# Kernel optimization log

Measured on AMD Instinct MI355X. Metric: run time of the kernel, lower is better.

## Reference

```python
import jax, jax.numpy as jnp
import numpy as np
import math

B, S, D, H, NL, DFF, C, K = 32, 1024, 512, 8, 6, 2048, 128, 8
HD = D // H  # head_dim = 64
EPS = 1e-5


def setup_inputs() -> dict:
    key = jax.random.key(0)
    ks = jax.random.split(key, 24)
    n = lambda k, shape, s=0.02: jax.random.normal(k, shape, jnp.float32) * s
    return {
        'theta': jax.random.uniform(ks[0], (B, S), jnp.float32, -math.pi, math.pi),
        'cond': jax.random.normal(ks[1], (B, C), jnp.float32),
        'attn_bias': jax.random.normal(ks[2], (H, S, S), jnp.float32) * 0.1,
        'embed_W': n(ks[3], (2, D)), 'embed_b': jnp.zeros((D,), jnp.float32),
        'ln1_g': jnp.ones((NL, D), jnp.float32), 'ln1_b': jnp.zeros((NL, D), jnp.float32),
        'ada1_W': n(ks[4], (NL, C, 2 * D)), 'ada1_b': jnp.zeros((NL, 2 * D), jnp.float32),
        'Wq': n(ks[5], (NL, D, D)), 'bq': jnp.zeros((NL, D), jnp.float32),
        'Wk': n(ks[6], (NL, D, D)), 'bk': jnp.zeros((NL, D), jnp.float32),
        'Wv': n(ks[7], (NL, D, D)), 'bv': jnp.zeros((NL, D), jnp.float32),
        'Wo': n(ks[8], (NL, D, D)), 'bo': jnp.zeros((NL, D), jnp.float32),
        'ln2_g': jnp.ones((NL, D), jnp.float32), 'ln2_b': jnp.zeros((NL, D), jnp.float32),
        'ada2_W': n(ks[9], (NL, C, 2 * D)), 'ada2_b': jnp.zeros((NL, 2 * D), jnp.float32),
        'W1': n(ks[10], (NL, D, DFF)), 'b1': jnp.zeros((NL, DFF), jnp.float32),
        'W2': n(ks[11], (NL, DFF, D)), 'b2': jnp.zeros((NL, D), jnp.float32),
        'fn_g': jnp.ones((D,), jnp.float32), 'fn_b': jnp.zeros((D,), jnp.float32),
        'head_W': n(ks[12], (D, 3 * K)), 'head_b': jnp.zeros((3 * K,), jnp.float32),
    }


def _layer_norm(x, g, b):
    m = jnp.mean(x, axis=-1, keepdims=True)
    v = jnp.mean(jnp.square(x - m), axis=-1, keepdims=True)
    return (x - m) * jax.lax.rsqrt(v + EPS) * g + b


def _adaln(x, cond, g, b, pW, pb):
    # AdaLN(x, c) = (1 + scale(c)) * LN(x) + shift(c)
    ss = cond @ pW + pb                      # [B, 2D]
    scale, shift = jnp.split(ss, 2, axis=-1)  # each [B, D]
    return (1.0 + scale[:, None, :]) * _layer_norm(x, g, b) + shift[:, None, :]


def reference(theta, cond, attn_bias, embed_W, embed_b, ln1_g, ln1_b, ada1_W, ada1_b,
              Wq, bq, Wk, bk, Wv, bv, Wo, bo, ln2_g, ln2_b, ada2_W, ada2_b,
              W1, b1, W2, b2, fn_g, fn_b, head_W, head_b):
    b_sz, s_len = theta.shape
    # circular embedding: (cos, sin) -> d_model
    emb_in = jnp.stack([jnp.cos(theta), jnp.sin(theta)], axis=-1)  # [B, S, 2]
    x = emb_in @ embed_W + embed_b                                 # [B, S, D]
    causal = jnp.triu(jnp.ones((s_len, s_len), bool), k=1)         # True above diag
    neg_inf = jnp.asarray(-jnp.inf, x.dtype)
    inv_sqrt = 1.0 / math.sqrt(HD)
    for i in range(NL):
        h = _adaln(x, cond, ln1_g[i], ln1_b[i], ada1_W[i], ada1_b[i])
        q = (h @ Wq[i] + bq[i]).reshape(b_sz, s_len, H, HD)
        k = (h @ Wk[i] + bk[i]).reshape(b_sz, s_len, H, HD)
        v = (h @ Wv[i] + bv[i]).reshape(b_sz, s_len, H, HD)
        scores = jnp.einsum('bqhd,bkhd->bhqk', q, k) * inv_sqrt  # [B, H, S, S]
        scores = scores + attn_bias[None]
        scores = jnp.where(causal[None, None], neg_inf, scores)
        attn = jax.nn.softmax(scores, axis=-1)
        ao = jnp.einsum('bhqk,bkhd->bqhd', attn, v).reshape(b_sz, s_len, D)
        x = x + (ao @ Wo[i] + bo[i])
        h2 = _adaln(x, cond, ln2_g[i], ln2_b[i], ada2_W[i], ada2_b[i])
        ff = jax.nn.gelu(h2 @ W1[i] + b1[i], approximate=False) @ W2[i] + b2[i]
        x = x + ff
    x = _layer_norm(x, fn_g, fn_b)
    return x @ head_W + head_b  # [B, S, 3K] mixture params (logw, mu, log-kappa)
```

## Files before the change

### kernel.cpp

```cpp
#include <hip/hip_runtime.h>


typedef short s8v __attribute__((ext_vector_type(8)));
typedef float f4v __attribute__((ext_vector_type(4)));
typedef unsigned u2v __attribute__((ext_vector_type(2)));
typedef unsigned u4v __attribute__((ext_vector_type(4)));

#define Q_SCALE 0.18033688011112042f
#define LOG2E   1.4426950408889634f

static __device__ __forceinline__ short f2bf(float f) {
  union { float f; unsigned u; } v; v.f = f;
  unsigned r = v.u + 0x7fffu + ((v.u >> 16) & 1u);
  return (short)(r >> 16);
}
static __device__ __forceinline__ float bf2f(unsigned short s) {
  union { unsigned u; float f; } v; v.u = ((unsigned)s) << 16;
  return v.f;
}
static __device__ __forceinline__ unsigned cvtpk(float lo, float hi) {
  unsigned r;
  asm("v_cvt_pk_bf16_f32 %0, %1, %2" : "=v"(r) : "v"(lo), "v"(hi));
  return r;
}
static __device__ __forceinline__ float fexp2(float x) {
  float r;
  asm("v_exp_f32 %0, %1" : "=v"(r) : "v"(x));
  return r;
}
static __device__ __forceinline__ void gl_lds16(const short* g, short* l) {
  __builtin_amdgcn_global_load_lds(
      (const __attribute__((address_space(1))) unsigned int*)g,
      (__attribute__((address_space(3))) unsigned int*)l, 16, 0, 0);
}

__global__ void transpose_all_k(const float* __restrict__ Wq, const float* __restrict__ Wk,
                                const float* __restrict__ Wv, const float* __restrict__ Wo,
                                const float* __restrict__ W1, const float* __restrict__ W2,
                                int l, short* __restrict__ wbf) {
  int id = blockIdx.x;
  const float* in; short* out; int K, N, tx, ty;
  if (id < 1024) {
    int m = id >> 8, t = id & 255;
    in = (m == 0 ? Wq : m == 1 ? Wk : m == 2 ? Wv : Wo) + (size_t)l * 262144;
    out = wbf + (size_t)m * 262144;
    K = 512; N = 512; tx = t & 15; ty = t >> 4;
  } else if (id < 2048) {
    int t = id - 1024;
    in = W1 + (size_t)l * 1048576; out = wbf + 1048576;
    K = 512; N = 2048; tx = t & 63; ty = t >> 6;
  } else {
    int t = id - 2048;
    in = W2 + (size_t)l * 1048576; out = wbf + 2097152;
    K = 2048; N = 512; tx = t & 15; ty = t >> 4;
  }
  __shared__ float tb[32][33];
  int n0 = tx * 32, k0 = ty * 32;
  int cx = threadIdx.x & 31, cy = threadIdx.x >> 5;
#pragma unroll
  for (int r = 0; r < 4; r++)
    tb[cy + r * 8][cx] = in[(size_t)(k0 + cy + r * 8) * N + n0 + cx];
  __syncthreads();
#pragma unroll
  for (int r = 0; r < 4; r++)
    out[(size_t)(n0 + cy + r * 8) * K + k0 + cx] = f2bf(tb[cx][cy + r * 8]);
}

__global__ void bias_cvt_k(const float* __restrict__ in, short* __restrict__ out) {
  int i = blockIdx.x * 256 + threadIdx.x;
  float4 v = ((const float4*)in)[i];
  ushort4 o;
  o.x = (unsigned short)f2bf(v.x * LOG2E);
  o.y = (unsigned short)f2bf(v.y * LOG2E);
  o.z = (unsigned short)f2bf(v.z * LOG2E);
  o.w = (unsigned short)f2bf(v.w * LOG2E);
  ((ushort4*)out)[i] = o;
}

__global__ void hwt_k(const float* __restrict__ hW, short* __restrict__ hWT) {
  int i = blockIdx.x * 256 + threadIdx.x;
  int n = i >> 9, k = i & 511;
  hWT[i] = (n < 24) ? f2bf(hW[(size_t)k * 24 + n]) : (short)0;
}

__global__ void concat_qkvb_k(const float* bq, const float* bk, const float* bv, float* out) {
  int l = blockIdx.x;
  for (int i = threadIdx.x; i < 1536; i += 256) {
    float v = (i < 512) ? bq[l * 512 + i] * Q_SCALE
            : (i < 1024 ? bk[l * 512 + i - 512] : bv[l * 512 + i - 1024]);
    out[l * 1536 + i] = v;
  }
}

__global__ void cond_proj_k(const float* __restrict__ cond,
                            const float* __restrict__ a1W, const float* __restrict__ a1b,
                            const float* __restrict__ a2W, const float* __restrict__ a2b,
                            float* __restrict__ ss) {
  int lw = blockIdx.y, which = lw & 1, l = lw >> 1;
  const float* W = (which ? a2W : a1W) + (size_t)l * 128 * 1024;
  const float* bb = (which ? a2b : a1b) + (size_t)l * 1024;
  __shared__ float cs[32 * 128];
  for (int i = threadIdx.x; i < 32 * 128; i += 256) cs[i] = cond[i];
  __syncthreads();
  int n = blockIdx.x * 256 + threadIdx.x;
  float bias = bb[n];
  for (int g = 0; g < 4; g++) {
    float acc[8];
#pragma unroll
    for (int i = 0; i < 8; i++) acc[i] = 0.f;
    for (int c = 0; c < 128; c++) {
      float w = W[(size_t)c * 1024 + n];
#pragma unroll
      for (int i = 0; i < 8; i++) acc[i] += cs[(g * 8 + i) * 128 + c] * w;
    }
#pragma unroll
    for (int i = 0; i < 8; i++)
      ss[((size_t)lw * 32 + g * 8 + i) * 1024 + n] = acc[i] + bias;
  }
}

__global__ void embed_k(const float* __restrict__ theta, const float* __restrict__ eW,
                        const float* __restrict__ eb, float* __restrict__ x) {
  int row = blockIdx.x * 4 + (threadIdx.x >> 6), lane = threadIdx.x & 63;
  float th = theta[row], sn, cn;
  sincosf(th, &sn, &cn);
  int d = lane * 8;
  float* xo = x + (size_t)row * 512 + d;
#pragma unroll
  for (int i = 0; i < 8; i++) xo[i] = cn * eW[d + i] + sn * eW[512 + d + i] + eb[d + i];
}

template<bool HASDEL>
__global__ void adaln_k(float* __restrict__ x, const short* delta,
                        const float* __restrict__ ss,
                        const float* __restrict__ g, const float* __restrict__ be,
                        short* h) {
  int row = blockIdx.x * 4 + (threadIdx.x >> 6), lane = threadIdx.x & 63;
  int b = row >> 10;
  float* xr = x + (size_t)row * 512 + lane * 8;
  float4 va = ((const float4*)xr)[0], vb = ((const float4*)xr)[1];
  float v[8] = {va.x, va.y, va.z, va.w, vb.x, vb.y, vb.z, vb.w};
  if (HASDEL) {
    s8v dv = *(const s8v*)(delta + (size_t)row * 512 + lane * 8);
#pragma unroll
    for (int i = 0; i < 8; i++) v[i] += bf2f((unsigned short)dv[i]);
    float4 o0 = {v[0], v[1], v[2], v[3]}, o1 = {v[4], v[5], v[6], v[7]};
    ((float4*)xr)[0] = o0; ((float4*)xr)[1] = o1;
  }
  float sm = 0.f;
#pragma unroll
  for (int i = 0; i < 8; i++) sm += v[i];
#pragma unroll
  for (int off = 1; off < 64; off <<= 1) sm += __shfl_xor(sm, off);
  float mean = sm * (1.f / 512.f);
  float sq = 0.f;
#pragma unroll
  for (int i = 0; i < 8; i++) { float d = v[i] - mean; sq += d * d; }
#pragma unroll
  for (int off = 1; off < 64; off <<= 1) sq += __shfl_xor(sq, off);
  float rs = rsqrtf(sq * (1.f / 512.f) + 1e-5f);
  const float* sb = ss + (size_t)b * 1024 + lane * 8;
  const float* gp = g + lane * 8;
  const float* bp = be + lane * 8;
  s8v o;
#pragma unroll
  for (int i = 0; i < 8; i++) {
    float xh = (v[i] - mean) * rs * gp[i] + bp[i];
    o[i] = f2bf((1.f + sb[i]) * xh + sb[i + 512]);
  }
  *(s8v*)(h + (size_t)row * 512 + lane * 8) = o;
}

__global__ void fln_k(const float* __restrict__ x, const short* delta,
                      const float* __restrict__ g, const float* __restrict__ be,
                      short* h) {
  int row = blockIdx.x * 4 + (threadIdx.x >> 6), lane = threadIdx.x & 63;
  const float* xr = x + (size_t)row * 512 + lane * 8;
  float4 va = ((const float4*)xr)[0], vb = ((const float4*)xr)[1];
  float v[8] = {va.x, va.y, va.z, va.w, vb.x, vb.y, vb.z, vb.w};
  s8v dv = *(const s8v*)(delta + (size_t)row * 512 + lane * 8);
#pragma unroll
  for (int i = 0; i < 8; i++) v[i] += bf2f((unsigned short)dv[i]);
  float sm = 0.f;
#pragma unroll
  for (int i = 0; i < 8; i++) sm += v[i];
#pragma unroll
  for (int off = 1; off < 64; off <<= 1) sm += __shfl_xor(sm, off);
  float mean = sm * (1.f / 512.f);
  float sq = 0.f;
#pragma unroll
  for (int i = 0; i < 8; i++) { float d = v[i] - mean; sq += d * d; }
#pragma unroll
  for (int off = 1; off < 64; off <<= 1) sq += __shfl_xor(sq, off);
  float rs = rsqrtf(sq * (1.f / 512.f) + 1e-5f);
  const float* gp = g + lane * 8;
  const float* bp = be + lane * 8;
  s8v o;
#pragma unroll
  for (int i = 0; i < 8; i++) o[i] = f2bf((v[i] - mean) * rs * gp[i] + bp[i]);
  *(s8v*)(h + (size_t)row * 512 + lane * 8) = o;
}

template<int EPI>
__global__ __launch_bounds__(256, 3) void gemm_r3_k(const short* __restrict__ A,
                                                    const short* __restrict__ BT,
                                                    const float* __restrict__ bias,
                                                    short* __restrict__ outb,
                                                    int N, int K) {
  __shared__ __align__(16) short lsA[3][4096];
  __shared__ __align__(16) short lsB[3][4096];
  int tid = threadIdx.x, lane = tid & 63, w = tid >> 6;
  int wm = w >> 1, wn = w & 1;
  int l15 = lane & 15, l4 = lane >> 4;
  int lrow = lane >> 2, lchunk = lane & 3;
  int poff = ((l15 << 2) + (l4 ^ ((l15 >> 1) & 3))) << 3;
  int nb = N >> 7;
  int bid = blockIdx.x;
  int xcd = bid & 7, rr = bid >> 3;
  int mloc = rr / nb, nidx = rr - mloc * nb;
  int m0 = (xcd * 32 + mloc) << 7, n0 = nidx << 7;

  f4v z4 = {0.f, 0.f, 0.f, 0.f};
  f4v acc[4][4];
#pragma unroll
  for (int i = 0; i < 4; i++)
#pragma unroll
    for (int j = 0; j < 4; j++) acc[i][j] = z4;

  int co = (lchunk ^ ((lrow >> 1) & 3)) << 3;

  auto STAGE = [&](int t) {
    int slot = t % 3;
    int ko = t << 5;
#pragma unroll
    for (int tt = 0; tt < 2; tt++) {
      int r0 = w * 32 + tt * 16;
      int row = r0 + lrow;
      gl_lds16(A + (size_t)(m0 + row) * K + ko + co, lsA[slot] + r0 * 32);
      gl_lds16(BT + (size_t)(n0 + row) * K + ko + co, lsB[slot] + r0 * 32);
    }
  };
  auto LOADF = [&](int t, s8v* af, s8v* bfr) {
    int slot = t % 3;
    const short* At = lsA[slot] + (wm * 4) * 512 + poff;
    const short* Bt = lsB[slot] + (wn * 4) * 512 + poff;
#pragma unroll
    for (int i = 0; i < 4; i++) {
      af[i] = *(const s8v*)(At + i * 512);
      bfr[i] = *(const s8v*)(Bt + i * 512);
    }
  };

  int NT = K >> 5;
  STAGE(0); STAGE(1);
  asm volatile("s_waitcnt vmcnt(4)" ::: "memory");
  __builtin_amdgcn_s_barrier();
  s8v af[4], bfr[4];
  LOADF(0, af, bfr);
  for (int t = 0; t < NT; ++t) {
    if (t + 2 < NT) STAGE(t + 2);
    __builtin_amdgcn_sched_barrier(0);
#pragma unroll
    for (int i = 0; i < 4; i++)
#pragma unroll
      for (int j = 0; j < 4; j++)
        acc[i][j] = __builtin_amdgcn_mfma_f32_16x16x32_bf16(af[i], bfr[j], acc[i][j], 0, 0, 0);
    if (t + 1 < NT) {
      if (t + 2 < NT) asm volatile("s_waitcnt vmcnt(4)" ::: "memory");
      else            asm volatile("s_waitcnt vmcnt(0)" ::: "memory");
      __builtin_amdgcn_s_barrier();
      LOADF(t + 1, af, bfr);
    }
  }
#pragma unroll
  for (int i = 0; i < 4; i++) {
    int gr0 = m0 + wm * 64 + i * 16 + l4 * 4;
#pragma unroll
    for (int j = 0; j < 4; j++) {
      int gc = n0 + wn * 64 + j * 16 + l15;
      float bv = bias[gc];
#pragma unroll
      for (int r = 0; r < 4; r++) {
        float v = acc[i][j][r] + bv;
        if (EPI == 1) {
          float tg = v * (-1.5957691216f - 0.0713548162726f * v * v);
          v = v / (1.f + __expf(tg));
        }
        outb[(size_t)(gr0 + r) * N + gc] = f2bf(v);
      }
    }
  }
}

__global__ __launch_bounds__(256) void qkvt_k(const short* __restrict__ A,
                                              const short* __restrict__ BT,
                                              const float* __restrict__ bias,
                                              short* __restrict__ qk,
                                              short* __restrict__ vtb) {
  __shared__ __align__(16) short lsA[2][4096];
  __shared__ __align__(16) short lsB[2][4096];
  int tid = threadIdx.x, lane = tid & 63, w = tid >> 6;
  int wm = w >> 1, wn = w & 1;
  int l15 = lane & 15, l4 = lane >> 4;
  int lrow = lane >> 2, lchunk = lane & 3;
  int poff = ((l15 << 2) + (l4 ^ ((l15 >> 1) & 3))) << 3;
  int bid = blockIdx.x;
  int xcd = bid & 7, rr = bid >> 3;
  int mloc = rr / 12, nidx = rr - mloc * 12;
  int m0 = (xcd * 32 + mloc) << 7, n0 = nidx << 7;
  bool isV = (n0 >= 1024);
  bool isQ = (n0 < 512);

  f4v z4 = {0.f, 0.f, 0.f, 0.f};
  f4v acc[4][4];
#pragma unroll
  for (int i = 0; i < 4; i++)
#pragma unroll
    for (int j = 0; j < 4; j++) acc[i][j] = z4;

  int co = (lchunk ^ ((lrow >> 1) & 3)) << 3;

  auto STAGE = [&](int t) {
    int slot = t & 1;
    int ko = t << 5;
#pragma unroll
    for (int tt = 0; tt < 2; tt++) {
      int r0 = w * 32 + tt * 16;
      int row = r0 + lrow;
      gl_lds16(A + (size_t)(m0 + row) * 512 + ko + co, lsA[slot] + r0 * 32);
      gl_lds16(BT + (size_t)(n0 + row) * 512 + ko + co, lsB[slot] + r0 * 32);
    }
  };

  const int NT = 16;
  STAGE(0);
  for (int t = 0; t < NT; ++t) {
    if (t + 1 < NT) {
      STAGE(t + 1);
      asm volatile("s_waitcnt vmcnt(4)" ::: "memory");
    } else {
      asm volatile("s_waitcnt vmcnt(0)" ::: "memory");
    }
    __builtin_amdgcn_s_barrier();
    int slot = t & 1;
    const short* At = lsA[slot] + (wm * 4) * 512 + poff;
    const short* Bt = lsB[slot] + (wn * 4) * 512 + poff;
    s8v af[4], bfr[4];
#pragma unroll
    for (int i = 0; i < 4; i++) {
      af[i] = *(const s8v*)(At + i * 512);
      bfr[i] = *(const s8v*)(Bt + i * 512);
    }
    if (!isV) {
#pragma unroll
      for (int i = 0; i < 4; i++)
#pragma unroll
        for (int j = 0; j < 4; j++)
          acc[i][j] = __builtin_amdgcn_mfma_f32_16x16x32_bf16(af[i], bfr[j], acc[i][j], 0, 0, 0);
    } else {
#pragma unroll
      for (int j = 0; j < 4; j++)
#pragma unroll
        for (int i = 0; i < 4; i++)
          acc[j][i] = __builtin_amdgcn_mfma_f32_16x16x32_bf16(bfr[j], af[i], acc[j][i], 0, 0, 0);
    }
    __builtin_amdgcn_s_barrier();
  }
  if (!isV) {
    float scl = isQ ? Q_SCALE : 1.f;
#pragma unroll
    for (int i = 0; i < 4; i++) {
      int gr0 = m0 + wm * 64 + i * 16 + l4 * 4;
#pragma unroll
      for (int j = 0; j < 4; j++) {
        int gc = n0 + wn * 64 + j * 16 + l15;
        float bv = bias[gc];
#pragma unroll
        for (int r = 0; r < 4; r++)
          qk[(size_t)(gr0 + r) * 1024 + gc] = f2bf(acc[i][j][r] * scl + bv);
      }
    }
  } else {
    int b = m0 >> 10, s0 = m0 & 1023;
#pragma unroll
    for (int j = 0; j < 4; j++) {
      int col = n0 + wn * 64 + j * 16 + l4 * 4;
#pragma unroll
      for (int i = 0; i < 4; i++) {
        int scol = s0 + wm * 64 + i * 16 + l15;
#pragma unroll
        for (int r = 0; r < 4; r++) {
          float v = acc[j][i][r] + bias[col + r];
          vtb[((size_t)b * 512 + col - 1024 + r) * 1024 + scol] = f2bf(v);
        }
      }
    }
  }
}

__global__ __launch_bounds__(256, 4) void attn_k(const short* __restrict__ qk,
                                                 const short* __restrict__ vt,
                                                 const short* __restrict__ biasNT,
                                                 short* __restrict__ ao) {
  __shared__ __align__(16) short Kl[2][64 * 64];
  __shared__ __align__(16) short Vl[2][64 * 64];
  int tid = threadIdx.x, lane = tid & 63, w = tid >> 6;
  int bid = blockIdx.x;
  int qt = 7 - (bid >> 8), b = (bid >> 3) & 31, h = bid & 7;
  int l15 = lane & 15, l4 = lane >> 4;
  int lrow = lane >> 3, lchunk = lane & 7;

  f4v z4 = {0.f, 0.f, 0.f, 0.f};
  s8v qf[2][2];
#pragma unroll
  for (int g = 0; g < 2; g++) {
    const short* qp = qk + (size_t)(b * 1024 + qt * 128 + g * 64 + w * 16 + l15) * 1024 + h * 64;
    qf[g][0] = *(const s8v*)(qp + l4 * 8);
    qf[g][1] = *(const s8v*)(qp + 32 + l4 * 8);
  }
  f4v o[2][4], lac[2];
#pragma unroll
  for (int g = 0; g < 2; g++) {
    lac[g] = z4;
#pragma unroll
    for (int j = 0; j < 4; j++) o[g][j] = z4;
  }
  s8v ones;
#pragma unroll
  for (int e = 0; e < 8; e++) ones[e] = (short)0x3F80;

  auto STAGE = [&](int buf, int kt) {
#pragma unroll
    for (int t = 0; t < 2; t++) {
      int r0 = (w * 2 + t) * 8;
      int row = r0 + lrow;
      gl_lds16(qk + (size_t)(b * 1024 + kt * 64 + row) * 1024 + 512 + h * 64 +
                   ((lchunk ^ (row & 7)) << 3),
               &Kl[buf][r0 * 64]);
      gl_lds16(vt + (size_t)(b * 512 + h * 64 + row) * 1024 + kt * 64 +
                   ((lchunk ^ (row & 7)) << 3),
               &Vl[buf][r0 * 64]);
    }
  };

  int nkt = 2 * qt + 2;
  STAGE(0, 0);
  for (int kt = 0; kt < nkt; kt++) {
    int cur = kt & 1;
    ushort4 bh[2][4];
#pragma unroll
    for (int g = 0; g < 2; g++) {
      if (kt > 2 * qt + g) continue;
      const short* bp = biasNT + ((size_t)h * 1024 + qt * 128 + g * 64 + w * 16 + l15) * 1024 +
                        kt * 64 + l4 * 4;
#pragma unroll
      for (int j = 0; j < 4; j++) bh[g][j] = *(const ushort4*)(bp + j * 16);
    }
    __builtin_amdgcn_sched_barrier(0);
    if (kt + 1 < nkt) {
      STAGE(cur ^ 1, kt + 1);
      asm volatile("s_waitcnt vmcnt(4)" ::: "memory");
    } else {
      asm volatile("s_waitcnt vmcnt(0)" ::: "memory");
    }
    __builtin_amdgcn_s_barrier();
    const short* Kc = &Kl[cur][0];
    const short* Vc = &Vl[cur][0];
#pragma unroll
    for (int g = 0; g < 2; g++) {
      int diag = 2 * qt + g;
      if (kt > diag) continue;
      f4v s[4];
      __builtin_amdgcn_s_setprio(1);
#pragma unroll
      for (int j = 0; j < 4; j++) {
        f4v bc;
        bc[0] = bf2f(bh[g][j].x); bc[1] = bf2f(bh[g][j].y);
        bc[2] = bf2f(bh[g][j].z); bc[3] = bf2f(bh[g][j].w);
        int kr = j * 16 + l15;
        s8v kf0 = *(const s8v*)(Kc + kr * 64 + ((l4 ^ (kr & 7)) << 3));
        s8v kf1 = *(const s8v*)(Kc + kr * 64 + (((l4 + 4) ^ (kr & 7)) << 3));
        s[j] = __builtin_amdgcn_mfma_f32_16x16x32_bf16(kf0, qf[g][0], bc, 0, 0, 0);
        s[j] = __builtin_amdgcn_mfma_f32_16x16x32_bf16(kf1, qf[g][1], s[j], 0, 0, 0);
      }
      __builtin_amdgcn_s_setprio(0);
      if (kt == diag) {
#pragma unroll
        for (int j = 0; j < 4; j++)
#pragma unroll
          for (int r = 0; r < 4; r++) {
            int kk = j * 16 + l4 * 4 + r, qq = w * 16 + l15;
            s[j][r] = (kk > qq) ? 0.f : fexp2(s[j][r]);
          }
      } else {
#pragma unroll
        for (int j = 0; j < 4; j++)
#pragma unroll
          for (int r = 0; r < 4; r++) s[j][r] = fexp2(s[j][r]);
      }
      unsigned X0[4], X1[4];
#pragma unroll
      for (int j = 0; j < 4; j++) {
        X0[j] = cvtpk(s[j][0], s[j][1]);
        X1[j] = cvtpk(s[j][2], s[j][3]);
      }
      u2v a0 = __builtin_amdgcn_permlane32_swap(X0[0], X0[1], false, false);
      u2v a1 = __builtin_amdgcn_permlane16_swap(a0[0], a0[1], false, false);
      u2v b0 = __builtin_amdgcn_permlane32_swap(X1[0], X1[1], false, false);
      u2v b1 = __builtin_amdgcn_permlane16_swap(b0[0], b0[1], false, false);
      u2v c0 = __builtin_amdgcn_permlane32_swap(X0[2], X0[3], false, false);
      u2v c1 = __builtin_amdgcn_permlane16_swap(c0[0], c0[1], false, false);
      u2v d0 = __builtin_amdgcn_permlane32_swap(X1[2], X1[3], false, false);
      u2v d1 = __builtin_amdgcn_permlane16_swap(d0[0], d0[1], false, false);
      u4v P0 = {a1[0], b1[0], a1[1], b1[1]};
      u4v P1 = {c1[0], d1[0], c1[1], d1[1]};
      s8v pf0 = __builtin_bit_cast(s8v, P0);
      s8v pf1 = __builtin_bit_cast(s8v, P1);
      __builtin_amdgcn_s_setprio(1);
      lac[g] = __builtin_amdgcn_mfma_f32_16x16x32_bf16(pf0, ones, lac[g], 0, 0, 0);
      lac[g] = __builtin_amdgcn_mfma_f32_16x16x32_bf16(pf1, ones, lac[g], 0, 0, 0);
#pragma unroll
      for (int j = 0; j < 4; j++) {
        int dr = j * 16 + l15;
        s8v vf0 = *(const s8v*)(Vc + dr * 64 + ((l4 ^ (dr & 7)) << 3));
        s8v vf1 = *(const s8v*)(Vc + dr * 64 + (((l4 + 4) ^ (dr & 7)) << 3));
        o[g][j] = __builtin_amdgcn_mfma_f32_16x16x32_bf16(pf0, vf0, o[g][j], 0, 0, 0);
        o[g][j] = __builtin_amdgcn_mfma_f32_16x16x32_bf16(pf1, vf1, o[g][j], 0, 0, 0);
      }
      __builtin_amdgcn_s_setprio(0);
    }
    __builtin_amdgcn_s_barrier();
  }
#pragma unroll
  for (int g = 0; g < 2; g++)
#pragma unroll
    for (int r = 0; r < 4; r++) {
      float rl = 1.f / lac[g][r];
      int qr = qt * 128 + g * 64 + w * 16 + l4 * 4 + r;
#pragma unroll
      for (int j = 0; j < 4; j++) {
        int d = j * 16 + l15;
        ao[(size_t)(b * 1024 + qr) * 512 + h * 64 + d] = f2bf(o[g][j][r] * rl);
      }
    }
}

__global__ __launch_bounds__(256) void head_k(const short* __restrict__ X,
                                              const short* __restrict__ hWT,
                                              const float* __restrict__ hb,
                                              float* __restrict__ out) {
  __shared__ __align__(16) short lA[128 * 64];
  int tid = threadIdx.x, lane = tid & 63, w = tid >> 6;
  int l15 = lane & 15, l4 = lane >> 4;
  int lrow = lane >> 3, lchunk = lane & 7;
  int m0 = blockIdx.x * 128;
  f4v z4 = {0.f, 0.f, 0.f, 0.f};
  f4v acc[2][2];
#pragma unroll
  for (int i = 0; i < 2; i++)
#pragma unroll
    for (int j = 0; j < 2; j++) acc[i][j] = z4;

  for (int k0 = 0; k0 < 512; k0 += 64) {
#pragma unroll
    for (int t = 0; t < 4; t++) {
      int r0 = (w * 4 + t) * 8;
      int row = r0 + lrow;
      gl_lds16(X + (size_t)(m0 + row) * 512 + k0 + ((lchunk ^ (row & 7)) << 3), lA + r0 * 64);
    }
    __syncthreads();
#pragma unroll
    for (int kk = 0; kk < 2; kk++) {
      s8v af[2], bfr[2];
#pragma unroll
      for (int i = 0; i < 2; i++) {
        int ra = w * 32 + i * 16 + l15;
        af[i] = *(const s8v*)(lA + ra * 64 + (((l4 + kk * 4) ^ (ra & 7)) << 3));
      }
#pragma unroll
      for (int j = 0; j < 2; j++)
        bfr[j] = *(const s8v*)(hWT + (size_t)(j * 16 + l15) * 512 + k0 + kk * 32 + l4 * 8);
#pragma unroll
      for (int i = 0; i < 2; i++)
#pragma unroll
        for (int j = 0; j < 2; j++)
          acc[i][j] = __builtin_amdgcn_mfma_f32_16x16x32_bf16(af[i], bfr[j], acc[i][j], 0, 0, 0);
    }
    __syncthreads();
  }
#pragma unroll
  for (int i = 0; i < 2; i++) {
#pragma unroll
    for (int j = 0; j < 2; j++) {
      int col = j * 16 + l15;
      if (col < 24) {
        float bv = hb[col];
#pragma unroll
        for (int r = 0; r < 4; r++) {
          int row = m0 + w * 32 + i * 16 + l4 * 4 + r;
          out[(size_t)row * 24 + col] = acc[i][j][r] + bv;
        }
      }
    }
  }
}

extern "C" void kernel_launch(void* const* d_in, const int* in_sizes, int n_in,
                              void* d_out, int out_size, void* d_ws, size_t ws_size,
                              hipStream_t stream) {
  (void)in_sizes; (void)n_in; (void)out_size;
  const float* theta   = (const float*)d_in[0];
  const float* cond    = (const float*)d_in[1];
  const float* attn_b  = (const float*)d_in[2];
  const float* embed_W = (const float*)d_in[3];
  const float* embed_b = (const float*)d_in[4];
  const float* ln1_g   = (const float*)d_in[5];
  const float* ln1_b   = (const float*)d_in[6];
  const float* ada1_W  = (const float*)d_in[7];
  const float* ada1_b  = (const float*)d_in[8];
  const float* Wq      = (const float*)d_in[9];
  const float* bq      = (const float*)d_in[10];
  const float* Wk      = (const float*)d_in[11];
  const float* bk      = (const float*)d_in[12];
  const float* Wv      = (const float*)d_in[13];
  const float* bv      = (const float*)d_in[14];
  const float* Wo      = (const float*)d_in[15];
  const float* bo      = (const float*)d_in[16];
  const float* ln2_g   = (const float*)d_in[17];
  const float* ln2_b   = (const float*)d_in[18];
  const float* ada2_W  = (const float*)d_in[19];
  const float* ada2_b  = (const float*)d_in[20];
  const float* W1      = (const float*)d_in[21];
  const float* b1      = (const float*)d_in[22];
  const float* W2      = (const float*)d_in[23];
  const float* b2      = (const float*)d_in[24];
  const float* fn_g    = (const float*)d_in[25];
  const float* fn_b    = (const float*)d_in[26];
  const float* head_W  = (const float*)d_in[27];
  const float* head_b  = (const float*)d_in[28];

  const size_t REQ = 242814976ull;
  const size_t REQ2 = 259592192ull;
  if (ws_size < REQ) return;
  bool bias_once = (ws_size >= REQ2);

  char* ws = (char*)d_ws;
  float* xw    = (float*)(ws + 0ull);
  short* qk    = (short*)(ws + 67108864ull);
  short* vtb   = (short*)(ws + 134217728ull);
  short* biasT = (short*)(ws + (bias_once ? 242814976ull : 167772160ull));
  short* qf    = (short*)(ws + 67108864ull);
  short* hbuf  = (short*)(ws + 201326592ull);
  short* wbf   = (short*)(ws + 234881024ull);
  float* ssb   = (float*)(ws + 241172480ull);
  float* bqkv  = (float*)(ws + 242745344ull);
  short* hWT   = (short*)(ws + 242782208ull);

  concat_qkvb_k<<<6, 256, 0, stream>>>(bq, bk, bv, bqkv);
  cond_proj_k<<<dim3(4, 12), 256, 0, stream>>>(cond, ada1_W, ada1_b, ada2_W, ada2_b, ssb);
  hwt_k<<<64, 256, 0, stream>>>(head_W, hWT);
  embed_k<<<8192, 256, 0, stream>>>(theta, embed_W, embed_b, xw);
  if (bias_once) bias_cvt_k<<<8192, 256, 0, stream>>>(attn_b, biasT);

  for (int l = 0; l < 6; l++) {
    transpose_all_k<<<3072, 256, 0, stream>>>(Wq, Wk, Wv, Wo, W1, W2, l, wbf);
    if (!bias_once) bias_cvt_k<<<8192, 256, 0, stream>>>(attn_b, biasT);

    if (l == 0)
      adaln_k<false><<<8192, 256, 0, stream>>>(xw, nullptr, ssb + (size_t)(l * 2) * 32768,
                                               ln1_g + l * 512, ln1_b + l * 512, hbuf);
    else
      adaln_k<true><<<8192, 256, 0, stream>>>(xw, hbuf, ssb + (size_t)(l * 2) * 32768,
                                              ln1_g + l * 512, ln1_b + l * 512, hbuf);
    qkvt_k<<<3072, 256, 0, stream>>>(hbuf, wbf, bqkv + l * 1536, qk, vtb);
    attn_k<<<2048, 256, 0, stream>>>(qk, vtb, biasT, hbuf);
    gemm_r3_k<0><<<1024, 256, 0, stream>>>(hbuf, wbf + 786432, bo + l * 512, vtb, 512, 512);
    adaln_k<true><<<8192, 256, 0, stream>>>(xw, vtb, ssb + (size_t)(l * 2 + 1) * 32768,
                                            ln2_g + l * 512, ln2_b + l * 512, hbuf);
    gemm_r3_k<1><<<4096, 256, 0, stream>>>(hbuf, wbf + 1048576, b1 + l * 2048, qf, 2048, 512);
    gemm_r3_k<0><<<1024, 256, 0, stream>>>(qf, wbf + 2097152, b2 + l * 512, hbuf, 512, 2048);
  }
  fln_k<<<8192, 256, 0, stream>>>(xw, hbuf, fn_g, fn_b, hbuf);
  head_k<<<256, 256, 0, stream>>>(hbuf, hWT, head_b, (float*)d_out);
}
```

Baseline: 2.744 ms.

## Split QKV projection into Q/K and V kernels with triple-buffered prefetch

The fused QKV projection kernel is split into two kernels. The Q/K kernel uses a three-slot LDS ring with register prefetch of the next tile's fragments, and its launch bounds ask for 3 blocks per CU. The V kernel keeps the old double-buffered loop with its transposed output, so neither kernel branches per block on the tile type. The s_setprio hints in the attention kernel are also removed. The cost is an extra launch, and the bigger LDS footprint may limit occupancy.

```diff
diff --git a/kernel.cpp b/kernel.cpp
--- a/kernel.cpp
+++ b/kernel.cpp
@@ -292,11 +292,94 @@
   }
 }
 
-__global__ __launch_bounds__(256) void qkvt_k(const short* __restrict__ A,
-                                              const short* __restrict__ BT,
-                                              const float* __restrict__ bias,
-                                              short* __restrict__ qk,
-                                              short* __restrict__ vtb) {
+__global__ __launch_bounds__(256, 3) void qk_proj_k(const short* __restrict__ A,
+                                                    const short* __restrict__ BT,
+                                                    const float* __restrict__ bias,
+                                                    short* __restrict__ qk) {
+  __shared__ __align__(16) short lsA[3][4096];
+  __shared__ __align__(16) short lsB[3][4096];
+  int tid = threadIdx.x, lane = tid & 63, w = tid >> 6;
+  int wm = w >> 1, wn = w & 1;
+  int l15 = lane & 15, l4 = lane >> 4;
+  int lrow = lane >> 2, lchunk = lane & 3;
+  int poff = ((l15 << 2) + (l4 ^ ((l15 >> 1) & 3))) << 3;
+  int bid = blockIdx.x;
+  int xcd = bid & 7, rr = bid >> 3;
+  int mloc = rr >> 3, nidx = rr & 7;
+  int m0 = (xcd * 32 + mloc) << 7, n0 = nidx << 7;
+  bool isQ = (n0 < 512);
+
+  f4v z4 = {0.f, 0.f, 0.f, 0.f};
+  f4v acc[4][4];
+#pragma unroll
+  for (int i = 0; i < 4; i++)
+#pragma unroll
+    for (int j = 0; j < 4; j++) acc[i][j] = z4;
+
+  int co = (lchunk ^ ((lrow >> 1) & 3)) << 3;
+
+  auto STAGE = [&](int t) {
+    int slot = t % 3;
+    int ko = t << 5;
+#pragma unroll
+    for (int tt = 0; tt < 2; tt++) {
+      int r0 = w * 32 + tt * 16;
+      int row = r0 + lrow;
+      gl_lds16(A + (size_t)(m0 + row) * 512 + ko + co, lsA[slot] + r0 * 32);
+      gl_lds16(BT + (size_t)(n0 + row) * 512 + ko + co, lsB[slot] + r0 * 32);
+    }
+  };
+  auto LOADF = [&](int t, s8v* af, s8v* bfr) {
+    int slot = t % 3;
+    const short* At = lsA[slot] + (wm * 4) * 512 + poff;
+    const short* Bt = lsB[slot] + (wn * 4) * 512 + poff;
+#pragma unroll
+    for (int i = 0; i < 4; i++) {
+      af[i] = *(const s8v*)(At + i * 512);
+      bfr[i] = *(const s8v*)(Bt + i * 512);
+    }
+  };
+
+  const int NT = 16;
+  STAGE(0); STAGE(1);
+  asm volatile("s_waitcnt vmcnt(4)" ::: "memory");
+  __builtin_amdgcn_s_barrier();
+  s8v af[4], bfr[4];
+  LOADF(0, af, bfr);
+  for (int t = 0; t < NT; ++t) {
+    if (t + 2 < NT) STAGE(t + 2);
+    __builtin_amdgcn_sched_barrier(0);
+#pragma unroll
+    for (int i = 0; i < 4; i++)
+#pragma unroll
+      for (int j = 0; j < 4; j++)
+        acc[i][j] = __builtin_amdgcn_mfma_f32_16x16x32_bf16(af[i], bfr[j], acc[i][j], 0, 0, 0);
+    if (t + 1 < NT) {
+      if (t + 2 < NT) asm volatile("s_waitcnt vmcnt(4)" ::: "memory");
+      else            asm volatile("s_waitcnt vmcnt(0)" ::: "memory");
+      __builtin_amdgcn_s_barrier();
+      LOADF(t + 1, af, bfr);
+    }
+  }
+  float scl = isQ ? Q_SCALE : 1.f;
+#pragma unroll
+  for (int i = 0; i < 4; i++) {
+    int gr0 = m0 + wm * 64 + i * 16 + l4 * 4;
+#pragma unroll
+    for (int j = 0; j < 4; j++) {
+      int gc = n0 + wn * 64 + j * 16 + l15;
+      float bv = bias[gc];
+#pragma unroll
+      for (int r = 0; r < 4; r++)
+        qk[(size_t)(gr0 + r) * 1024 + gc] = f2bf(acc[i][j][r] * scl + bv);
+    }
+  }
+}
+
+__global__ __launch_bounds__(256) void v_proj_k(const short* __restrict__ A,
+                                                const short* __restrict__ BT,
+                                                const float* __restrict__ bias,
+                                                short* __restrict__ vtb) {
   __shared__ __align__(16) short lsA[2][4096];
   __shared__ __align__(16) short lsB[2][4096];
   int tid = threadIdx.x, lane = tid & 63, w = tid >> 6;
@@ -306,10 +389,8 @@
   int poff = ((l15 << 2) + (l4 ^ ((l15 >> 1) & 3))) << 3;
   int bid = blockIdx.x;
   int xcd = bid & 7, rr = bid >> 3;
-  int mloc = rr / 12, nidx = rr - mloc * 12;
-  int m0 = (xcd * 32 + mloc) << 7, n0 = nidx << 7;
-  bool isV = (n0 >= 1024);
-  bool isQ = (n0 < 512);
+  int mloc = rr >> 2, nidx = rr & 3;
+  int m0 = (xcd * 32 + mloc) << 7, n0 = 1024 + (nidx << 7);
 
   f4v z4 = {0.f, 0.f, 0.f, 0.f};
   f4v acc[4][4];
@@ -351,48 +432,24 @@
       af[i] = *(const s8v*)(At + i * 512);
       bfr[i] = *(const s8v*)(Bt + i * 512);
     }
-    if (!isV) {
+#pragma unroll
+    for (int j = 0; j < 4; j++)
 #pragma unroll
       for (int i = 0; i < 4; i++)
-#pragma unroll
-        for (int j = 0; j < 4; j++)
-          acc[i][j] = __builtin_amdgcn_mfma_f32_16x16x32_bf16(af[i], bfr[j], acc[i][j], 0, 0, 0);
-    } else {
-#pragma unroll
-      for (int j = 0; j < 4; j++)
-#pragma unroll
-        for (int i = 0; i < 4; i++)
-          acc[j][i] = __builtin_amdgcn_mfma_f32_16x16x32_bf16(bfr[j], af[i], acc[j][i], 0, 0, 0);
-    }
+        acc[j][i] = __builtin_amdgcn_mfma_f32_16x16x32_bf16(bfr[j], af[i], acc[j][i], 0, 0, 0);
     __builtin_amdgcn_s_barrier();
   }
-  if (!isV) {
-    float scl = isQ ? Q_SCALE : 1.f;
+  int b = m0 >> 10, s0 = m0 & 1023;
+#pragma unroll
+  for (int j = 0; j < 4; j++) {
+    int col = n0 + wn * 64 + j * 16 + l4 * 4;
 #pragma unroll
     for (int i = 0; i < 4; i++) {
-      int gr0 = m0 + wm * 64 + i * 16 + l4 * 4;
-#pragma unroll
-      for (int j = 0; j < 4; j++) {
-        int gc = n0 + wn * 64 + j * 16 + l15;
-        float bv = bias[gc];
-#pragma unroll
-        for (int r = 0; r < 4; r++)
-          qk[(size_t)(gr0 + r) * 1024 + gc] = f2bf(acc[i][j][r] * scl + bv);
-      }
-    }
-  } else {
-    int b = m0 >> 10, s0 = m0 & 1023;
-#pragma unroll
-    for (int j = 0; j < 4; j++) {
-      int col = n0 + wn * 64 + j * 16 + l4 * 4;
-#pragma unroll
-      for (int i = 0; i < 4; i++) {
-        int scol = s0 + wm * 64 + i * 16 + l15;
-#pragma unroll
-        for (int r = 0; r < 4; r++) {
-          float v = acc[j][i][r] + bias[col + r];
-          vtb[((size_t)b * 512 + col - 1024 + r) * 1024 + scol] = f2bf(v);
-        }
+      int scol = s0 + wm * 64 + i * 16 + l15;
+#pragma unroll
+      for (int r = 0; r < 4; r++) {
+        float v = acc[j][i][r] + bias[col + r];
+        vtb[((size_t)b * 512 + col - 1024 + r) * 1024 + scol] = f2bf(v);
       }
     }
   }
@@ -471,7 +528,6 @@
       int diag = 2 * qt + g;
       if (kt > diag) continue;
       f4v s[4];
-      __builtin_amdgcn_s_setprio(1);
 #pragma unroll
       for (int j = 0; j < 4; j++) {
         f4v bc;
@@ -483,7 +539,6 @@
         s[j] = __builtin_amdgcn_mfma_f32_16x16x32_bf16(kf0, qf[g][0], bc, 0, 0, 0);
         s[j] = __builtin_amdgcn_mfma_f32_16x16x32_bf16(kf1, qf[g][1], s[j], 0, 0, 0);
       }
-      __builtin_amdgcn_s_setprio(0);
       if (kt == diag) {
 #pragma unroll
         for (int j = 0; j < 4; j++)
@@ -516,7 +571,6 @@
       u4v P1 = {c1[0], d1[0], c1[1], d1[1]};
       s8v pf0 = __builtin_bit_cast(s8v, P0);
       s8v pf1 = __builtin_bit_cast(s8v, P1);
-      __builtin_amdgcn_s_setprio(1);
       lac[g] = __builtin_amdgcn_mfma_f32_16x16x32_bf16(pf0, ones, lac[g], 0, 0, 0);
       lac[g] = __builtin_amdgcn_mfma_f32_16x16x32_bf16(pf1, ones, lac[g], 0, 0, 0);
 #pragma unroll
@@ -527,7 +581,6 @@
         o[g][j] = __builtin_amdgcn_mfma_f32_16x16x32_bf16(pf0, vf0, o[g][j], 0, 0, 0);
         o[g][j] = __builtin_amdgcn_mfma_f32_16x16x32_bf16(pf1, vf1, o[g][j], 0, 0, 0);
       }
-      __builtin_amdgcn_s_setprio(0);
     }
     __builtin_amdgcn_s_barrier();
   }
@@ -672,7 +725,8 @@
     else
       adaln_k<true><<<8192, 256, 0, stream>>>(xw, hbuf, ssb + (size_t)(l * 2) * 32768,
                                               ln1_g + l * 512, ln1_b + l * 512, hbuf);
-    qkvt_k<<<3072, 256, 0, stream>>>(hbuf, wbf, bqkv + l * 1536, qk, vtb);
+    qk_proj_k<<<2048, 256, 0, stream>>>(hbuf, wbf, bqkv + l * 1536, qk);
+    v_proj_k<<<1024, 256, 0, stream>>>(hbuf, wbf, bqkv + l * 1536, vtb);
     attn_k<<<2048, 256, 0, stream>>>(qk, vtb, biasT, hbuf);
     gemm_r3_k<0><<<1024, 256, 0, stream>>>(hbuf, wbf + 786432, bo + l * 512, vtb, 512, 512);
     adaln_k<true><<<8192, 256, 0, stream>>>(xw, vtb, ssb + (size_t)(l * 2 + 1) * 32768,
```

Result: no change. 2.718 ms (-0.9%).
